# Performance work log

Measured on AMD Instinct MI355X. Metric: run time of the kernel, lower is better.

## Reference

```python
import jax, jax.numpy as jnp
import numpy as np

N_HEAD = 12
LN_EPS = 1e-5


def setup_inputs() -> dict:
    key = jax.random.key(0)
    ks = jax.random.split(key, 4)
    B, T, C = 4, 2048, 768
    s = C ** -0.5
    return {
        "x": jax.random.normal(ks[0], (B, T, C), jnp.float32),
        "w_attn": jax.random.normal(ks[1], (C, 3 * C), jnp.float32) * s,
        "b_attn": jnp.zeros((3 * C,), jnp.float32),
        "w_proj": jax.random.normal(ks[2], (C, C), jnp.float32) * s,
        "b_proj": jnp.zeros((C,), jnp.float32),
        "ln1_g": jnp.ones((C,), jnp.float32),
        "ln1_b": jnp.zeros((C,), jnp.float32),
        "ln2_g": jnp.ones((C,), jnp.float32),
        "ln2_b": jnp.zeros((C,), jnp.float32),
    }


def _layernorm(x, g, b):
    mu = jnp.mean(x, axis=-1, keepdims=True)
    var = jnp.mean(jnp.square(x - mu), axis=-1, keepdims=True)
    return (x - mu) * jax.lax.rsqrt(var + LN_EPS) * g + b


def _attn(h, w_attn, b_attn, w_proj, b_proj):
    B, T, C = h.shape
    hd = C // N_HEAD
    # Faithful to torch: view(B,T,H,3*hd) then split 3*hd -> q,k,v per head
    qkv = (h @ w_attn + b_attn).reshape(B, T, N_HEAD, 3, hd)
    q = jnp.transpose(qkv[:, :, :, 0, :], (0, 2, 1, 3))  # (B,H,T,hd)
    k = jnp.transpose(qkv[:, :, :, 1, :], (0, 2, 1, 3))
    v = jnp.transpose(qkv[:, :, :, 2, :], (0, 2, 1, 3))
    # NOTE: scale is C**-0.5 (full embed dim) and there is NO causal mask,
    # exactly as in the source.
    scores = jnp.einsum("bhtd,bhsd->bhts", q, k) * (C ** -0.5)
    a = jax.nn.softmax(scores, axis=-1)
    y = jnp.einsum("bhts,bhsd->bhtd", a, v)
    y = jnp.transpose(y, (0, 2, 1, 3)).reshape(B, T, C)
    return y @ w_proj + b_proj


def reference(x, w_attn, b_attn, w_proj, b_proj, ln1_g, ln1_b, ln2_g, ln2_b):
    # Faithful to source Block.forward: attn applied twice, MLP never called.
    x = x + _attn(_layernorm(x, ln1_g, ln1_b), w_attn, b_attn, w_proj, b_proj)
    x = x + _attn(_layernorm(x, ln2_g, ln2_b), w_attn, b_attn, w_proj, b_proj)
    return x
```

## Files before the change

### kernel.cpp

```cpp
#include <hip/hip_runtime.h>


using bf16x8 = __attribute__((ext_vector_type(8))) short;
using f32x4  = __attribute__((ext_vector_type(4))) float;

__device__ __forceinline__ unsigned short f2b(float f) {
  unsigned u = __builtin_bit_cast(unsigned, f);
  u += 0x7FFFu + ((u >> 16) & 1u);
  return (unsigned short)(u >> 16);
}

#define ASYNC16(g, l)                                                        \
  __builtin_amdgcn_global_load_lds(                                          \
      (const __attribute__((address_space(1))) void*)(g),                    \
      (__attribute__((address_space(3))) void*)(l), 16, 0, 0)

__global__ __launch_bounds__(256) void wt_kernel(const float* __restrict__ w,
                                                 unsigned short* __restrict__ wt,
                                                 int N) {
  __shared__ float tile[32][33];
  const int n0 = blockIdx.x * 32, k0 = blockIdx.y * 32;
  const int tx = threadIdx.x, ty = threadIdx.y;
#pragma unroll
  for (int i = 0; i < 32; i += 8)
    tile[ty + i][tx] = w[(size_t)(k0 + ty + i) * N + n0 + tx];
  __syncthreads();
#pragma unroll
  for (int i = 0; i < 32; i += 8)
    wt[(size_t)(n0 + ty + i) * 768 + k0 + tx] = f2b(tile[tx][ty + i]);
}

__global__ __launch_bounds__(256) void ln_kernel(const float* __restrict__ x,
                                                 const float* __restrict__ g,
                                                 const float* __restrict__ b,
                                                 unsigned short* __restrict__ h) {
  __shared__ float red[8];
  const int row = blockIdx.x;
  const int tid = threadIdx.x;
  const float* xr = x + (size_t)row * 768;
  float v0 = xr[tid], v1 = xr[tid + 256], v2 = xr[tid + 512];
  float s = v0 + v1 + v2;
  float s2 = v0 * v0 + v1 * v1 + v2 * v2;
#pragma unroll
  for (int off = 1; off < 64; off <<= 1) {
    s += __shfl_xor(s, off);
    s2 += __shfl_xor(s2, off);
  }
  if ((tid & 63) == 0) { red[tid >> 6] = s; red[4 + (tid >> 6)] = s2; }
  __syncthreads();
  const float S  = red[0] + red[1] + red[2] + red[3];
  const float S2 = red[4] + red[5] + red[6] + red[7];
  const float mu  = S * (1.0f / 768.0f);
  const float var = S2 * (1.0f / 768.0f) - mu * mu;
  const float inv = rsqrtf(var + 1e-5f);
  unsigned short* hr = h + (size_t)row * 768;
  hr[tid]       = f2b((v0 - mu) * inv * g[tid] + b[tid]);
  hr[tid + 256] = f2b((v1 - mu) * inv * g[tid + 256] + b[tid + 256]);
  hr[tid + 512] = f2b((v2 - mu) * inv * g[tid + 512] + b[tid + 512]);
}

template <int EPI>
__global__ __launch_bounds__(256, 2) void gemm_kernel(
    const unsigned short* __restrict__ A, const unsigned short* __restrict__ Bt,
    const float* __restrict__ bias, const float* __restrict__ resid,
    unsigned short* __restrict__ q, unsigned short* __restrict__ k,
    unsigned short* __restrict__ v, float* __restrict__ outF) {
  __shared__ alignas(16) unsigned short As[128 * 32];
  __shared__ alignas(16) unsigned short Bs[128 * 32];

  const int tid = threadIdx.x;
  const int wv = tid >> 6;
  const int lane = tid & 63;
  const int quad = lane >> 4;
  const int l15 = lane & 15;
  const int m0 = blockIdx.y * 128;
  const int n0 = blockIdx.x * 128;

  const int o0 = wv * 1024 + lane * 16;
  const int rT0 = o0 >> 6, c0 = (o0 & 63) >> 1;
  const int o1 = o0 + 4096;
  const int rT1 = o1 >> 6, c1 = (o1 & 63) >> 1;

  const unsigned short* gA0 = A + (size_t)(m0 + rT0) * 768 + c0;
  const unsigned short* gA1 = A + (size_t)(m0 + rT1) * 768 + c1;
  const unsigned short* gB0 = Bt + (size_t)(n0 + rT0) * 768 + c0;
  const unsigned short* gB1 = Bt + (size_t)(n0 + rT1) * 768 + c1;
  unsigned short* lA0 = &As[wv * 512];
  unsigned short* lA1 = &As[wv * 512 + 2048];
  unsigned short* lB0 = &Bs[wv * 512];
  unsigned short* lB1 = &Bs[wv * 512 + 2048];

  f32x4 acc[4][4];
#pragma unroll
  for (int i = 0; i < 4; ++i)
#pragma unroll
    for (int j = 0; j < 4; ++j) acc[i][j] = {0.f, 0.f, 0.f, 0.f};

  const int mBase = (wv >> 1) * 64;
  const int nBase = (wv & 1) * 64;

  for (int kk = 0; kk < 24; ++kk) {
    const int ko = kk * 32;
    ASYNC16(gA0 + ko, lA0);
    ASYNC16(gA1 + ko, lA1);
    ASYNC16(gB0 + ko, lB0);
    ASYNC16(gB1 + ko, lB1);
    __syncthreads();
    bf16x8 af[4], bfv[4];
#pragma unroll
    for (int mt = 0; mt < 4; ++mt)
      af[mt] = *(const bf16x8*)&As[(mBase + mt * 16 + l15) * 32 + quad * 8];
#pragma unroll
    for (int nt = 0; nt < 4; ++nt)
      bfv[nt] = *(const bf16x8*)&Bs[(nBase + nt * 16 + l15) * 32 + quad * 8];
#pragma unroll
    for (int mt = 0; mt < 4; ++mt)
#pragma unroll
      for (int nt = 0; nt < 4; ++nt)
        acc[mt][nt] = __builtin_amdgcn_mfma_f32_16x16x32_bf16(af[mt], bfv[nt],
                                                              acc[mt][nt], 0, 0, 0);
    __syncthreads();
  }

  if constexpr (EPI == 0) {
#pragma unroll
    for (int mt = 0; mt < 4; ++mt) {
#pragma unroll
      for (int nt = 0; nt < 4; ++nt) {
        const int n = n0 + nBase + nt * 16 + l15;
        const int head = n / 192;
        const int rem = n - head * 192;
        const int sel = rem >> 6;
        const int d = rem & 63;
        unsigned short* tgt = (sel == 0) ? q : (sel == 1) ? k : v;
        const float bv = bias[n];
#pragma unroll
        for (int r = 0; r < 4; ++r) {
          const int m = m0 + mBase + mt * 16 + quad * 4 + r;
          const int bb = m >> 11;
          const int t = m & 2047;
          tgt[(((size_t)bb * 12 + head) * 2048 + t) * 64 + d] =
              f2b(acc[mt][nt][r] + bv);
        }
      }
    }
  } else {
#pragma unroll
    for (int mt = 0; mt < 4; ++mt) {
#pragma unroll
      for (int nt = 0; nt < 4; ++nt) {
        const int n = n0 + nBase + nt * 16 + l15;
        const float bv = bias[n];
#pragma unroll
        for (int r = 0; r < 4; ++r) {
          const int m = m0 + mBase + mt * 16 + quad * 4 + r;
          const size_t idx = (size_t)m * 768 + n;
          outF[idx] = resid[idx] + bv + acc[mt][nt][r];
        }
      }
    }
  }
}

__global__ __launch_bounds__(256) void vtrans_kernel(const unsigned short* __restrict__ V,
                                                     unsigned short* __restrict__ Vt) {
  const int bh = blockIdx.x;
  const int t = blockIdx.y * 256 + threadIdx.x;
  const uint4* s4 = (const uint4*)(V + ((size_t)bh * 2048 + t) * 64);
  const size_t ob = (size_t)bh * 64 * 2048 + t;
#pragma unroll
  for (int i = 0; i < 8; ++i) {
    const uint4 u = s4[i];
    const unsigned w[4] = {u.x, u.y, u.z, u.w};
#pragma unroll
    for (int j = 0; j < 4; ++j) {
      Vt[ob + (size_t)(i * 8 + j * 2) * 2048]     = (unsigned short)(w[j] & 0xFFFFu);
      Vt[ob + (size_t)(i * 8 + j * 2 + 1) * 2048] = (unsigned short)(w[j] >> 16);
    }
  }
}

#define PAD 68
__global__ __launch_bounds__(256, 3) void attn_kernel(
    const unsigned short* __restrict__ Q, const unsigned short* __restrict__ Km,
    const unsigned short* __restrict__ Vt, unsigned short* __restrict__ Y) {
  __shared__ alignas(16) unsigned short Ks[2][64 * PAD];
  __shared__ alignas(16) unsigned short Vs[2][64 * PAD];
  __shared__ alignas(16) unsigned short Ps[4][32 * PAD];

  const int bh = blockIdx.x;
  const int qt = blockIdx.y;
  const int tid = threadIdx.x;
  const int wv = tid >> 6;
  const int lane = tid & 63;
  const int quad = lane >> 4;
  const int l15 = lane & 15;
  const size_t bhT = (size_t)bh * 2048;

  bf16x8 qf[2][2];
#pragma unroll
  for (int mt = 0; mt < 2; ++mt) {
    const unsigned short* qb = Q + (bhT + qt * 128 + mt * 64 + wv * 16 + l15) * 64;
    qf[mt][0] = *(const bf16x8*)(qb + quad * 8);
    qf[mt][1] = *(const bf16x8*)(qb + 32 + quad * 8);
  }

  f32x4 o[2][4], ol[2];
#pragma unroll
  for (int mt = 0; mt < 2; ++mt) {
    ol[mt] = {0.f, 0.f, 0.f, 0.f};
#pragma unroll
    for (int nt = 0; nt < 4; ++nt) o[mt][nt] = {0.f, 0.f, 0.f, 0.f};
  }
  const bf16x8 ones = {0x3F80, 0x3F80, 0x3F80, 0x3F80,
                       0x3F80, 0x3F80, 0x3F80, 0x3F80};

  const int kr = tid >> 3;
  const int kc = (tid & 7) * 8;
  const unsigned short* gK = Km + (bhT + kr) * 64 + kc;
  const unsigned short* gV = Vt + ((size_t)bh * 64 + kr) * 2048 + kc;
  const int lo0 = kr * PAD + kc;
  const int lo1 = (kr + 32) * PAD + kc;
  const float c2 = 0.052062786090587f;

  bf16x8 sk0 = *(const bf16x8*)(gK);
  bf16x8 sk1 = *(const bf16x8*)(gK + 32 * 64);
  bf16x8 sv0 = *(const bf16x8*)(gV);
  bf16x8 sv1 = *(const bf16x8*)(gV + 32 * 2048);

  for (int c = 0; c < 32; ++c) {
    const int p = c & 1;
    *(bf16x8*)&Ks[p][lo0] = sk0;
    *(bf16x8*)&Ks[p][lo1] = sk1;
    *(bf16x8*)&Vs[p][lo0] = sv0;
    *(bf16x8*)&Vs[p][lo1] = sv1;
    __syncthreads();
    if (c < 31) {
      sk0 = *(const bf16x8*)(gK + (size_t)(c + 1) * 4096);
      sk1 = *(const bf16x8*)(gK + (size_t)(c + 1) * 4096 + 2048);
      sv0 = *(const bf16x8*)(gV + (c + 1) * 64);
      sv1 = *(const bf16x8*)(gV + (c + 1) * 64 + 32 * 2048);
    }

    f32x4 s[2][4];
#pragma unroll
    for (int nt = 0; nt < 4; ++nt) {
      s[0][nt] = {0.f, 0.f, 0.f, 0.f};
      s[1][nt] = {0.f, 0.f, 0.f, 0.f};
#pragma unroll
      for (int ks = 0; ks < 2; ++ks) {
        bf16x8 kf = *(const bf16x8*)&Ks[p][(nt * 16 + l15) * PAD + ks * 32 + quad * 8];
        s[0][nt] = __builtin_amdgcn_mfma_f32_16x16x32_bf16(qf[0][ks], kf, s[0][nt], 0, 0, 0);
        s[1][nt] = __builtin_amdgcn_mfma_f32_16x16x32_bf16(qf[1][ks], kf, s[1][nt], 0, 0, 0);
      }
    }

#pragma unroll
    for (int mt = 0; mt < 2; ++mt)
#pragma unroll
      for (int nt = 0; nt < 4; ++nt)
#pragma unroll
        for (int r = 0; r < 4; ++r) {
          const float pv = __builtin_amdgcn_exp2f(s[mt][nt][r] * c2);
          Ps[wv][(mt * 16 + quad * 4 + r) * PAD + nt * 16 + l15] =
              (unsigned short)(__builtin_bit_cast(unsigned, pv) >> 16);
        }

#pragma unroll
    for (int ks = 0; ks < 2; ++ks) {
      bf16x8 pf0 = *(const bf16x8*)&Ps[wv][(l15) * PAD + ks * 32 + quad * 8];
      bf16x8 pf1 = *(const bf16x8*)&Ps[wv][(16 + l15) * PAD + ks * 32 + quad * 8];
      ol[0] = __builtin_amdgcn_mfma_f32_16x16x32_bf16(pf0, ones, ol[0], 0, 0, 0);
      ol[1] = __builtin_amdgcn_mfma_f32_16x16x32_bf16(pf1, ones, ol[1], 0, 0, 0);
#pragma unroll
      for (int nt = 0; nt < 4; ++nt) {
        bf16x8 vf = *(const bf16x8*)&Vs[p][(nt * 16 + l15) * PAD + ks * 32 + quad * 8];
        o[0][nt] = __builtin_amdgcn_mfma_f32_16x16x32_bf16(pf0, vf, o[0][nt], 0, 0, 0);
        o[1][nt] = __builtin_amdgcn_mfma_f32_16x16x32_bf16(pf1, vf, o[1][nt], 0, 0, 0);
      }
    }
  }

  const int b = bh / 12;
  const int head = bh - b * 12;
#pragma unroll
  for (int mt = 0; mt < 2; ++mt) {
    const int qrow0 = qt * 128 + mt * 64 + wv * 16 + quad * 4;
#pragma unroll
    for (int r = 0; r < 4; ++r) {
      const float rl = 1.0f / ol[mt][r];
#pragma unroll
      for (int nt = 0; nt < 4; ++nt)
        Y[((size_t)(b * 2048 + qrow0 + r)) * 768 + head * 64 + nt * 16 + l15] =
            f2b(o[mt][nt][r] * rl);
    }
  }
}

extern "C" void kernel_launch(void* const* d_in, const int* in_sizes, int n_in,
                              void* d_out, int out_size, void* d_ws, size_t ws_size,
                              hipStream_t stream) {
  const float* x      = (const float*)d_in[0];
  const float* w_attn = (const float*)d_in[1];
  const float* b_attn = (const float*)d_in[2];
  const float* w_proj = (const float*)d_in[3];
  const float* b_proj = (const float*)d_in[4];
  const float* ln_g[2] = {(const float*)d_in[5], (const float*)d_in[7]};
  const float* ln_b[2] = {(const float*)d_in[6], (const float*)d_in[8]};
  float* out = (float*)d_out;

  unsigned short* wAt = (unsigned short*)d_ws;
  unsigned short* wPt = wAt + 2304 * 768;
  unsigned short* h   = wPt + 768 * 768;
  unsigned short* q   = h + 8192 * 768;
  unsigned short* k   = q + 48 * 2048 * 64;
  unsigned short* v   = k + 48 * 2048 * 64;
  unsigned short* vt  = v + 48 * 2048 * 64;
  unsigned short* y   = vt + 48 * 2048 * 64;

  wt_kernel<<<dim3(72, 24), dim3(32, 8), 0, stream>>>(w_attn, wAt, 2304);
  wt_kernel<<<dim3(24, 24), dim3(32, 8), 0, stream>>>(w_proj, wPt, 768);

  for (int pass = 0; pass < 2; ++pass) {
    const float* xin = pass ? (const float*)out : x;
    ln_kernel<<<8192, 256, 0, stream>>>(xin, ln_g[pass], ln_b[pass], h);
    gemm_kernel<0><<<dim3(18, 64), 256, 0, stream>>>(h, wAt, b_attn, nullptr,
                                                     q, k, v, nullptr);
    vtrans_kernel<<<dim3(48, 8), 256, 0, stream>>>(v, vt);
    attn_kernel<<<dim3(48, 16), 256, 0, stream>>>(q, k, vt, y);
    gemm_kernel<1><<<dim3(6, 64), 256, 0, stream>>>(y, wPt, b_proj, xin,
                                                    nullptr, nullptr, nullptr, out);
  }
}
```

Before: 414.3 us.

## Load K/V fragments directly from global memory, dropping LDS staging and barriers

```diff
diff --git a/kernel.cpp b/kernel.cpp
--- a/kernel.cpp
+++ b/kernel.cpp
@@ -184,8 +184,6 @@
 __global__ __launch_bounds__(256, 3) void attn_kernel(
     const unsigned short* __restrict__ Q, const unsigned short* __restrict__ Km,
     const unsigned short* __restrict__ Vt, unsigned short* __restrict__ Y) {
-  __shared__ alignas(16) unsigned short Ks[2][64 * PAD];
-  __shared__ alignas(16) unsigned short Vs[2][64 * PAD];
   __shared__ alignas(16) unsigned short Ps[4][32 * PAD];
 
   const int bh = blockIdx.x;
@@ -215,32 +213,24 @@
   const bf16x8 ones = {0x3F80, 0x3F80, 0x3F80, 0x3F80,
                        0x3F80, 0x3F80, 0x3F80, 0x3F80};
 
-  const int kr = tid >> 3;
-  const int kc = (tid & 7) * 8;
-  const unsigned short* gK = Km + (bhT + kr) * 64 + kc;
-  const unsigned short* gV = Vt + ((size_t)bh * 64 + kr) * 2048 + kc;
-  const int lo0 = kr * PAD + kc;
-  const int lo1 = (kr + 32) * PAD + kc;
+  const unsigned short* kc = Km + bhT * 64 + l15 * 64 + quad * 8;
+  const unsigned short* vc = Vt + ((size_t)bh * 64 + l15) * 2048 + quad * 8;
   const float c2 = 0.052062786090587f;
 
-  bf16x8 sk0 = *(const bf16x8*)(gK);
-  bf16x8 sk1 = *(const bf16x8*)(gK + 32 * 64);
-  bf16x8 sv0 = *(const bf16x8*)(gV);
-  bf16x8 sv1 = *(const bf16x8*)(gV + 32 * 2048);
-
   for (int c = 0; c < 32; ++c) {
-    const int p = c & 1;
-    *(bf16x8*)&Ks[p][lo0] = sk0;
-    *(bf16x8*)&Ks[p][lo1] = sk1;
-    *(bf16x8*)&Vs[p][lo0] = sv0;
-    *(bf16x8*)&Vs[p][lo1] = sv1;
-    __syncthreads();
-    if (c < 31) {
-      sk0 = *(const bf16x8*)(gK + (size_t)(c + 1) * 4096);
-      sk1 = *(const bf16x8*)(gK + (size_t)(c + 1) * 4096 + 2048);
-      sv0 = *(const bf16x8*)(gV + (c + 1) * 64);
-      sv1 = *(const bf16x8*)(gV + (c + 1) * 64 + 32 * 2048);
-    }
+    bf16x8 kf[4][2], vf[4][2];
+#pragma unroll
+    for (int nt = 0; nt < 4; ++nt)
+#pragma unroll
+      for (int ks = 0; ks < 2; ++ks)
+        kf[nt][ks] = *(const bf16x8*)(kc + nt * 1024 + ks * 32);
+#pragma unroll
+    for (int nt = 0; nt < 4; ++nt)
+#pragma unroll
+      for (int ks = 0; ks < 2; ++ks)
+        vf[nt][ks] = *(const bf16x8*)(vc + nt * 16 * 2048 + ks * 32);
+    kc += 4096;
+    vc += 64;
 
     f32x4 s[2][4];
 #pragma unroll
@@ -249,9 +239,8 @@
       s[1][nt] = {0.f, 0.f, 0.f, 0.f};
 #pragma unroll
       for (int ks = 0; ks < 2; ++ks) {
-        bf16x8 kf = *(const bf16x8*)&Ks[p][(nt * 16 + l15) * PAD + ks * 32 + quad * 8];
-        s[0][nt] = __builtin_amdgcn_mfma_f32_16x16x32_bf16(qf[0][ks], kf, s[0][nt], 0, 0, 0);
-        s[1][nt] = __builtin_amdgcn_mfma_f32_16x16x32_bf16(qf[1][ks], kf, s[1][nt], 0, 0, 0);
+        s[0][nt] = __builtin_amdgcn_mfma_f32_16x16x32_bf16(qf[0][ks], kf[nt][ks], s[0][nt], 0, 0, 0);
+        s[1][nt] = __builtin_amdgcn_mfma_f32_16x16x32_bf16(qf[1][ks], kf[nt][ks], s[1][nt], 0, 0, 0);
       }
     }
 
@@ -274,9 +263,8 @@
       ol[1] = __builtin_amdgcn_mfma_f32_16x16x32_bf16(pf1, ones, ol[1], 0, 0, 0);
 #pragma unroll
       for (int nt = 0; nt < 4; ++nt) {
-        bf16x8 vf = *(const bf16x8*)&Vs[p][(nt * 16 + l15) * PAD + ks * 32 + quad * 8];
-        o[0][nt] = __builtin_amdgcn_mfma_f32_16x16x32_bf16(pf0, vf, o[0][nt], 0, 0, 0);
-        o[1][nt] = __builtin_amdgcn_mfma_f32_16x16x32_bf16(pf1, vf, o[1][nt], 0, 0, 0);
+        o[0][nt] = __builtin_amdgcn_mfma_f32_16x16x32_bf16(pf0, vf[nt][ks], o[0][nt], 0, 0, 0);
+        o[1][nt] = __builtin_amdgcn_mfma_f32_16x16x32_bf16(pf1, vf[nt][ks], o[1][nt], 0, 0, 0);
       }
     }
   }
```

After: 606.6 us. +46.4%, slower.

## Transpose attention MFMA operands so P and Y are written as packed vectors

Applied to the files above, without the earlier changes.

```diff
diff --git a/kernel.cpp b/kernel.cpp
--- a/kernel.cpp
+++ b/kernel.cpp
@@ -8,6 +8,13 @@
   unsigned u = __builtin_bit_cast(unsigned, f);
   u += 0x7FFFu + ((u >> 16) & 1u);
   return (unsigned short)(u >> 16);
+}
+__device__ __forceinline__ unsigned pk2(float a, float b) {
+  unsigned ua = __builtin_bit_cast(unsigned, a);
+  ua += 0x7FFFu + ((ua >> 16) & 1u);
+  unsigned ub = __builtin_bit_cast(unsigned, b);
+  ub += 0x7FFFu + ((ub >> 16) & 1u);
+  return (ua >> 16) | (ub & 0xFFFF0000u);
 }
 
 #define ASYNC16(g, l)                                                        \
@@ -199,19 +206,19 @@
 
   bf16x8 qf[2][2];
 #pragma unroll
-  for (int mt = 0; mt < 2; ++mt) {
-    const unsigned short* qb = Q + (bhT + qt * 128 + mt * 64 + wv * 16 + l15) * 64;
-    qf[mt][0] = *(const bf16x8*)(qb + quad * 8);
-    qf[mt][1] = *(const bf16x8*)(qb + 32 + quad * 8);
-  }
-
-  f32x4 o[2][4], ol[2];
-#pragma unroll
-  for (int mt = 0; mt < 2; ++mt) {
-    ol[mt] = {0.f, 0.f, 0.f, 0.f};
-#pragma unroll
-    for (int nt = 0; nt < 4; ++nt) o[mt][nt] = {0.f, 0.f, 0.f, 0.f};
-  }
+  for (int g = 0; g < 2; ++g) {
+    const unsigned short* qb = Q + (bhT + qt * 128 + wv * 32 + g * 16 + l15) * 64;
+    qf[g][0] = *(const bf16x8*)(qb + quad * 8);
+    qf[g][1] = *(const bf16x8*)(qb + 32 + quad * 8);
+  }
+
+  f32x4 o[4][2], ol[2];
+#pragma unroll
+  for (int dt = 0; dt < 4; ++dt)
+#pragma unroll
+    for (int g = 0; g < 2; ++g) o[dt][g] = {0.f, 0.f, 0.f, 0.f};
+  ol[0] = {0.f, 0.f, 0.f, 0.f};
+  ol[1] = {0.f, 0.f, 0.f, 0.f};
   const bf16x8 ones = {0x3F80, 0x3F80, 0x3F80, 0x3F80,
                        0x3F80, 0x3F80, 0x3F80, 0x3F80};
 
@@ -244,39 +251,42 @@
 
     f32x4 s[2][4];
 #pragma unroll
-    for (int nt = 0; nt < 4; ++nt) {
-      s[0][nt] = {0.f, 0.f, 0.f, 0.f};
-      s[1][nt] = {0.f, 0.f, 0.f, 0.f};
-#pragma unroll
-      for (int ks = 0; ks < 2; ++ks) {
-        bf16x8 kf = *(const bf16x8*)&Ks[p][(nt * 16 + l15) * PAD + ks * 32 + quad * 8];
-        s[0][nt] = __builtin_amdgcn_mfma_f32_16x16x32_bf16(qf[0][ks], kf, s[0][nt], 0, 0, 0);
-        s[1][nt] = __builtin_amdgcn_mfma_f32_16x16x32_bf16(qf[1][ks], kf, s[1][nt], 0, 0, 0);
+    for (int tt = 0; tt < 4; ++tt) {
+      bf16x8 kf0 = *(const bf16x8*)&Ks[p][(tt * 16 + l15) * PAD + quad * 8];
+      bf16x8 kf1 = *(const bf16x8*)&Ks[p][(tt * 16 + l15) * PAD + 32 + quad * 8];
+      s[0][tt] = {0.f, 0.f, 0.f, 0.f};
+      s[1][tt] = {0.f, 0.f, 0.f, 0.f};
+      s[0][tt] = __builtin_amdgcn_mfma_f32_16x16x32_bf16(kf0, qf[0][0], s[0][tt], 0, 0, 0);
+      s[1][tt] = __builtin_amdgcn_mfma_f32_16x16x32_bf16(kf0, qf[1][0], s[1][tt], 0, 0, 0);
+      s[0][tt] = __builtin_amdgcn_mfma_f32_16x16x32_bf16(kf1, qf[0][1], s[0][tt], 0, 0, 0);
+      s[1][tt] = __builtin_amdgcn_mfma_f32_16x16x32_bf16(kf1, qf[1][1], s[1][tt], 0, 0, 0);
+    }
+
+#pragma unroll
+    for (int g = 0; g < 2; ++g)
+#pragma unroll
+      for (int tt = 0; tt < 4; ++tt) {
+        const float e0 = __builtin_amdgcn_exp2f(s[g][tt][0] * c2);
+        const float e1 = __builtin_amdgcn_exp2f(s[g][tt][1] * c2);
+        const float e2 = __builtin_amdgcn_exp2f(s[g][tt][2] * c2);
+        const float e3 = __builtin_amdgcn_exp2f(s[g][tt][3] * c2);
+        const unsigned long long pk =
+            (unsigned long long)pk2(e0, e1) |
+            ((unsigned long long)pk2(e2, e3) << 32);
+        *(unsigned long long*)&Ps[wv][(g * 16 + l15) * PAD + tt * 16 + quad * 4] = pk;
       }
-    }
-
-#pragma unroll
-    for (int mt = 0; mt < 2; ++mt)
-#pragma unroll
-      for (int nt = 0; nt < 4; ++nt)
-#pragma unroll
-        for (int r = 0; r < 4; ++r) {
-          const float pv = __builtin_amdgcn_exp2f(s[mt][nt][r] * c2);
-          Ps[wv][(mt * 16 + quad * 4 + r) * PAD + nt * 16 + l15] =
-              (unsigned short)(__builtin_bit_cast(unsigned, pv) >> 16);
-        }
 
 #pragma unroll
     for (int ks = 0; ks < 2; ++ks) {
       bf16x8 pf0 = *(const bf16x8*)&Ps[wv][(l15) * PAD + ks * 32 + quad * 8];
       bf16x8 pf1 = *(const bf16x8*)&Ps[wv][(16 + l15) * PAD + ks * 32 + quad * 8];
-      ol[0] = __builtin_amdgcn_mfma_f32_16x16x32_bf16(pf0, ones, ol[0], 0, 0, 0);
-      ol[1] = __builtin_amdgcn_mfma_f32_16x16x32_bf16(pf1, ones, ol[1], 0, 0, 0);
-#pragma unroll
-      for (int nt = 0; nt < 4; ++nt) {
-        bf16x8 vf = *(const bf16x8*)&Vs[p][(nt * 16 + l15) * PAD + ks * 32 + quad * 8];
-        o[0][nt] = __builtin_amdgcn_mfma_f32_16x16x32_bf16(pf0, vf, o[0][nt], 0, 0, 0);
-        o[1][nt] = __builtin_amdgcn_mfma_f32_16x16x32_bf16(pf1, vf, o[1][nt], 0, 0, 0);
+      ol[0] = __builtin_amdgcn_mfma_f32_16x16x32_bf16(ones, pf0, ol[0], 0, 0, 0);
+      ol[1] = __builtin_amdgcn_mfma_f32_16x16x32_bf16(ones, pf1, ol[1], 0, 0, 0);
+#pragma unroll
+      for (int dt = 0; dt < 4; ++dt) {
+        bf16x8 vf = *(const bf16x8*)&Vs[p][(dt * 16 + l15) * PAD + ks * 32 + quad * 8];
+        o[dt][0] = __builtin_amdgcn_mfma_f32_16x16x32_bf16(vf, pf0, o[dt][0], 0, 0, 0);
+        o[dt][1] = __builtin_amdgcn_mfma_f32_16x16x32_bf16(vf, pf1, o[dt][1], 0, 0, 0);
       }
     }
   }
@@ -284,15 +294,16 @@
   const int b = bh / 12;
   const int head = bh - b * 12;
 #pragma unroll
-  for (int mt = 0; mt < 2; ++mt) {
-    const int qrow0 = qt * 128 + mt * 64 + wv * 16 + quad * 4;
-#pragma unroll
-    for (int r = 0; r < 4; ++r) {
-      const float rl = 1.0f / ol[mt][r];
-#pragma unroll
-      for (int nt = 0; nt < 4; ++nt)
-        Y[((size_t)(b * 2048 + qrow0 + r)) * 768 + head * 64 + nt * 16 + l15] =
-            f2b(o[mt][nt][r] * rl);
+  for (int g = 0; g < 2; ++g) {
+    const float rl = 1.0f / ol[g][0];
+    const int row = qt * 128 + wv * 32 + g * 16 + l15;
+    unsigned short* yb = Y + ((size_t)(b * 2048 + row)) * 768 + head * 64;
+#pragma unroll
+    for (int dt = 0; dt < 4; ++dt) {
+      const unsigned long long pk =
+          (unsigned long long)pk2(o[dt][g][0] * rl, o[dt][g][1] * rl) |
+          ((unsigned long long)pk2(o[dt][g][2] * rl, o[dt][g][3] * rl) << 32);
+      *(unsigned long long*)(yb + dt * 16 + quad * 4) = pk;
     }
   }
 }
```

Result: no change. 410.3 us (-1.0%).
